# Performance work log

Hardware: AMD Instinct MI355X
Metric: run time of the kernel (lower is better)

The kernel has to match this reference:

```python
import jax, jax.numpy as jnp
import numpy as np

KERNEL = 2
STRIDE = 2
N_QUBITS = 4
N_LAYERS = 2
PI = np.float32(np.pi)
EPS = np.float32(1e-8)


def setup_inputs() -> dict:
    key = jax.random.key(0)
    k1, k2, k3, k4 = jax.random.split(key, 4)
    x = jax.random.normal(k1, (64, 3, 512, 512), dtype=jnp.float32)
    weights = jax.random.normal(k2, (N_LAYERS, N_QUBITS, 3), dtype=jnp.float32) * 0.1
    proj_w = jax.random.normal(k3, (4, N_QUBITS, 1, 1), dtype=jnp.float32) * 0.5
    proj_b = jax.random.normal(k4, (4,), dtype=jnp.float32) * 0.1
    return {"x": x, "weights": weights, "proj_w": proj_w, "proj_b": proj_b}


def _extract_patches(x):
    # x: (B, C, H, W) -> flattened 2x2 patches of grayscale image: (B, Ho, Wo, 4)
    B, C, H, W = x.shape
    Ho = (H - KERNEL) // STRIDE + 1
    Wo = (W - KERNEL) // STRIDE + 1
    x_gray = x.mean(axis=1)  # (B, H, W)
    # stride == kernel, so non-overlapping patches via reshape
    p = x_gray.reshape(B, Ho, KERNEL, Wo, KERNEL)
    p = p.transpose(0, 1, 3, 2, 4).reshape(B, Ho, Wo, KERNEL * KERNEL)
    return p


def reference(x, weights, proj_w, proj_b):
    patches = _extract_patches(x)  # (B, Ho, Wo, 4)
    # global min-max normalization (matches patches.min()/max() over whole tensor)
    pmin = patches.min()
    pmax = patches.max()
    patches = (patches - pmin) / (pmax - pmin + EPS)

    # simplified quantum simulation, fully vectorized over (B, Ho, Wo)
    encoded = jnp.sin(patches * PI)  # (B, Ho, Wo, Q)
    for layer in range(N_LAYERS):
        w = weights[layer]  # (Q, 3)
        neighbor = jnp.roll(encoded, shift=-1, axis=-1)  # encoded[(i+1)%Q]
        mixed = encoded * jnp.cos(w[:, 0]) + neighbor * jnp.sin(w[:, 1]) + w[:, 2]
        encoded = jnp.tanh(mixed)

    # (B, Ho, Wo, Q) -> (B, Q, Ho, Wo), then 1x1 conv projection
    q = encoded.transpose(0, 3, 1, 2)
    out = jnp.einsum('bqhw,oq->bohw', q, proj_w[:, :, 0, 0]) + proj_b[None, :, None, None]
    return out
```

## Files before the change

### kernel.cpp

```cpp
#include <hip/hip_runtime.h>
#include <hip/hip_fp16.h>

constexpr int BN = 64, CH = 3, HH = 512, WW = 512;
constexpr int HO = 256, WO = 256;
constexpr int HW = HH * WW;
constexpr int HOWO = HO * WO;
constexpr float EPS_F = 1e-8f;

constexpr int TPB = 256;
constexpr int GROUPS = BN * HO * (WO / 4);
constexpr int ABLOCKS = 2048;
constexpr int AT = ABLOCKS * TPB;
constexpr int AITERS = GROUPS / AT;
constexpr int CBLOCKS = GROUPS / TPB;

constexpr size_t GRAY_HALFS = (size_t)GROUPS * 16;

__device__ __forceinline__ float fast_tanh(float x) {
    float t = __builtin_amdgcn_exp2f(x * 2.8853900817779268f);
    return 1.0f - 2.0f * __builtin_amdgcn_rcpf(t + 1.0f);
}

__global__ __launch_bounds__(TPB) void k_pass1(const float* __restrict__ x,
                                               float4* __restrict__ gray4,
                                               float* __restrict__ part) {
    const int tid = blockIdx.x * TPB + threadIdx.x;
    const float c13 = 1.0f / 3.0f;
    float vmin = __int_as_float(0x7F800000);
    float vmax = __int_as_float(0xFF800000);

    #pragma unroll
    for (int it = 0; it < AITERS; ++it) {
        int grp = it * AT + tid;
        int b   = grp >> 14;
        int rem = grp & 16383;
        int ho  = rem >> 6;
        int wp  = rem & 63;
        const float* base = x + b * (CH * HW) + (2 * ho) * WW + 8 * wp;

        float row0[8], row1[8];
        #pragma unroll
        for (int c = 0; c < CH; ++c) {
            const float* pc = base + c * HW;
            float4 u0 = *(const float4*)(pc);
            float4 u1 = *(const float4*)(pc + 4);
            float4 v0 = *(const float4*)(pc + WW);
            float4 v1 = *(const float4*)(pc + WW + 4);
            float uu[8] = {u0.x, u0.y, u0.z, u0.w, u1.x, u1.y, u1.z, u1.w};
            float vv[8] = {v0.x, v0.y, v0.z, v0.w, v1.x, v1.y, v1.z, v1.w};
            if (c == 0) {
                #pragma unroll
                for (int k = 0; k < 8; ++k) { row0[k] = uu[k]; row1[k] = vv[k]; }
            } else {
                #pragma unroll
                for (int k = 0; k < 8; ++k) { row0[k] += uu[k]; row1[k] += vv[k]; }
            }
        }
        #pragma unroll
        for (int k = 0; k < 8; ++k) {
            row0[k] *= c13; row1[k] *= c13;
            vmin = fminf(vmin, fminf(row0[k], row1[k]));
            vmax = fmaxf(vmax, fmaxf(row0[k], row1[k]));
        }
        alignas(16) __half2 h2[8];
        #pragma unroll
        for (int p = 0; p < 4; ++p) {
            h2[2 * p]     = __floats2half2_rn(row0[2 * p], row0[2 * p + 1]);
            h2[2 * p + 1] = __floats2half2_rn(row1[2 * p], row1[2 * p + 1]);
        }
        gray4[(size_t)grp * 2]     = *(const float4*)&h2[0];
        gray4[(size_t)grp * 2 + 1] = *(const float4*)&h2[4];
    }

    #pragma unroll
    for (int off = 32; off > 0; off >>= 1) {
        vmin = fminf(vmin, __shfl_down(vmin, off, 64));
        vmax = fmaxf(vmax, __shfl_down(vmax, off, 64));
    }
    __shared__ float sm[8];
    int lane = threadIdx.x & 63, wid = threadIdx.x >> 6;
    if (lane == 0) { sm[wid] = vmin; sm[4 + wid] = vmax; }
    __syncthreads();
    if (threadIdx.x == 0) {
        part[2 * blockIdx.x]     = fminf(fminf(sm[0], sm[1]), fminf(sm[2], sm[3]));
        part[2 * blockIdx.x + 1] = fmaxf(fmaxf(sm[4], sm[5]), fmaxf(sm[6], sm[7]));
    }
}

__global__ __launch_bounds__(TPB) void k_reduce(const float* __restrict__ part,
                                                float* __restrict__ mm) {
    float m = __int_as_float(0x7F800000);
    float M = __int_as_float(0xFF800000);
    #pragma unroll
    for (int i = 0; i < ABLOCKS / TPB; ++i) {
        int j = i * TPB + threadIdx.x;
        m = fminf(m, part[2 * j]);
        M = fmaxf(M, part[2 * j + 1]);
    }
    #pragma unroll
    for (int off = 32; off > 0; off >>= 1) {
        m = fminf(m, __shfl_down(m, off, 64));
        M = fmaxf(M, __shfl_down(M, off, 64));
    }
    __shared__ float sm[8];
    int lane = threadIdx.x & 63, wid = threadIdx.x >> 6;
    if (lane == 0) { sm[wid] = m; sm[4 + wid] = M; }
    __syncthreads();
    if (threadIdx.x == 0) {
        mm[0] = fminf(fminf(sm[0], sm[1]), fminf(sm[2], sm[3]));
        mm[1] = fmaxf(fmaxf(sm[4], sm[5]), fmaxf(sm[6], sm[7]));
    }
}

__global__ __launch_bounds__(TPB) void k_main(const float4* __restrict__ gray4,
                                              const float* __restrict__ wts,
                                              const float* __restrict__ pw,
                                              const float* __restrict__ pb,
                                              const float* __restrict__ mm,
                                              float* __restrict__ out) {
    int grp = blockIdx.x * TPB + threadIdx.x;
    int b   = grp >> 14;
    int rem = grp & 16383;
    int ho  = rem >> 6;
    int wp  = rem & 63;

    float pmin   = mm[0];
    float sscale = 0.5f / (mm[1] - pmin + EPS_F);

    const float inv2pi = 0.15915494309189535f;
    float c0[2][4], s1[2][4], b2[2][4];
    #pragma unroll
    for (int l = 0; l < 2; ++l)
        #pragma unroll
        for (int q = 0; q < 4; ++q) {
            c0[l][q] = __builtin_amdgcn_cosf(wts[(l * 4 + q) * 3 + 0] * inv2pi);
            s1[l][q] = __builtin_amdgcn_sinf(wts[(l * 4 + q) * 3 + 1] * inv2pi);
            b2[l][q] = wts[(l * 4 + q) * 3 + 2];
        }
    float pwr[4][4], pbr[4];
    #pragma unroll
    for (int o = 0; o < 4; ++o) {
        pbr[o] = pb[o];
        #pragma unroll
        for (int q = 0; q < 4; ++q) pwr[o][q] = pw[o * 4 + q];
    }

    alignas(16) __half2 h2[8];
    *(float4*)&h2[0] = gray4[(size_t)grp * 2];
    *(float4*)&h2[4] = gray4[(size_t)grp * 2 + 1];

    float e[4][4];
    #pragma unroll
    for (int p = 0; p < 4; ++p) {
        e[p][0] = __low2float(h2[2 * p]);     e[p][1] = __high2float(h2[2 * p]);
        e[p][2] = __low2float(h2[2 * p + 1]); e[p][3] = __high2float(h2[2 * p + 1]);
    }
    #pragma unroll
    for (int p = 0; p < 4; ++p)
        #pragma unroll
        for (int q = 0; q < 4; ++q)
            e[p][q] = __builtin_amdgcn_sinf((e[p][q] - pmin) * sscale);
    #pragma unroll
    for (int l = 0; l < 2; ++l)
        #pragma unroll
        for (int p = 0; p < 4; ++p) {
            float mq[4];
            #pragma unroll
            for (int q = 0; q < 4; ++q)
                mq[q] = e[p][q] * c0[l][q] + e[p][(q + 1) & 3] * s1[l][q] + b2[l][q];
            #pragma unroll
            for (int q = 0; q < 4; ++q) e[p][q] = fast_tanh(mq[q]);
        }

    float* ob = out + b * (4 * HOWO) + ho * WO + 4 * wp;
    #pragma unroll
    for (int o = 0; o < 4; ++o) {
        float4 v;
        float* vp = &v.x;
        #pragma unroll
        for (int p = 0; p < 4; ++p) {
            float acc = pbr[o];
            #pragma unroll
            for (int q = 0; q < 4; ++q) acc += e[p][q] * pwr[o][q];
            vp[p] = acc;
        }
        *(float4*)(ob + o * HOWO) = v;
    }
}

extern "C" void kernel_launch(void* const* d_in, const int* in_sizes, int n_in,
                              void* d_out, int out_size, void* d_ws, size_t ws_size,
                              hipStream_t stream) {
    const float* x   = (const float*)d_in[0];
    const float* wts = (const float*)d_in[1];
    const float* pw  = (const float*)d_in[2];
    const float* pb  = (const float*)d_in[3];
    float* out = (float*)d_out;

    float4* gray4 = (float4*)d_ws;
    float*  part  = (float*)((char*)d_ws + GRAY_HALFS * sizeof(__half));
    float*  mm    = part + 2 * ABLOCKS;

    k_pass1 <<<ABLOCKS, TPB, 0, stream>>>(x, gray4, part);
    k_reduce<<<1,       TPB, 0, stream>>>(part, mm);
    k_main  <<<CBLOCKS, TPB, 0, stream>>>(gray4, wts, pw, pb, mm, out);
}
```

Measured before the change: 313.3 us.

## Fuse all passes into one cooperative persistent kernel holding gray values in registers

Replaces the three-kernel pipeline with a single cooperative kernel of 1024 blocks. Each thread keeps its fp16 grayscale patches in registers across a grid-wide sync, then finishes the global min/max reduction and computes the output. This removes the round trip of the grayscale intermediate through global memory and two kernel launches. The costs are higher register pressure (FITERS=4 groups of 8 half2 per thread), a grid barrier, and needing all 1024 blocks co-resident; the old three-kernel path is kept as a fallback if the cooperative launch fails.

```diff
diff --git a/kernel.cpp b/kernel.cpp
--- a/kernel.cpp
+++ b/kernel.cpp
@@ -1,5 +1,8 @@
 #include <hip/hip_runtime.h>
 #include <hip/hip_fp16.h>
+#include <hip/hip_cooperative_groups.h>
+
+namespace cg = cooperative_groups;
 
 constexpr int BN = 64, CH = 3, HH = 512, WW = 512;
 constexpr int HO = 256, WO = 256;
@@ -9,16 +12,174 @@
 
 constexpr int TPB = 256;
 constexpr int GROUPS = BN * HO * (WO / 4);
+
+constexpr int FBLK = 1024;
+constexpr int FTHR = FBLK * TPB;
+constexpr int FITERS = GROUPS / FTHR;
+
 constexpr int ABLOCKS = 2048;
 constexpr int AT = ABLOCKS * TPB;
 constexpr int AITERS = GROUPS / AT;
 constexpr int CBLOCKS = GROUPS / TPB;
-
 constexpr size_t GRAY_HALFS = (size_t)GROUPS * 16;
 
 __device__ __forceinline__ float fast_tanh(float x) {
     float t = __builtin_amdgcn_exp2f(x * 2.8853900817779268f);
     return 1.0f - 2.0f * __builtin_amdgcn_rcpf(t + 1.0f);
+}
+
+__global__ __launch_bounds__(TPB, 4) void k_fused(const float* __restrict__ x,
+                                                  const float* __restrict__ wts,
+                                                  const float* __restrict__ pw,
+                                                  const float* __restrict__ pb,
+                                                  float* __restrict__ part,
+                                                  float* __restrict__ out) {
+    const int tid = blockIdx.x * TPB + threadIdx.x;
+    const float c13 = 1.0f / 3.0f;
+    float vmin = __int_as_float(0x7F800000);
+    float vmax = __int_as_float(0xFF800000);
+
+    __half2 g[FITERS][8];
+
+    #pragma unroll
+    for (int it = 0; it < FITERS; ++it) {
+        const int grp = it * FTHR + tid;
+        const int b   = grp >> 14;
+        const int rem = grp & 16383;
+        const int ho  = rem >> 6;
+        const int wp  = rem & 63;
+        const float* base = x + b * (CH * HW) + (2 * ho) * WW + 8 * wp;
+
+        float row0[8], row1[8];
+        #pragma unroll
+        for (int c = 0; c < CH; ++c) {
+            const float* pc = base + c * HW;
+            float4 u0 = *(const float4*)(pc);
+            float4 u1 = *(const float4*)(pc + 4);
+            float4 v0 = *(const float4*)(pc + WW);
+            float4 v1 = *(const float4*)(pc + WW + 4);
+            float uu[8] = {u0.x, u0.y, u0.z, u0.w, u1.x, u1.y, u1.z, u1.w};
+            float vv[8] = {v0.x, v0.y, v0.z, v0.w, v1.x, v1.y, v1.z, v1.w};
+            if (c == 0) {
+                #pragma unroll
+                for (int k = 0; k < 8; ++k) { row0[k] = uu[k]; row1[k] = vv[k]; }
+            } else {
+                #pragma unroll
+                for (int k = 0; k < 8; ++k) { row0[k] += uu[k]; row1[k] += vv[k]; }
+            }
+        }
+        #pragma unroll
+        for (int k = 0; k < 8; ++k) {
+            row0[k] *= c13; row1[k] *= c13;
+            vmin = fminf(vmin, fminf(row0[k], row1[k]));
+            vmax = fmaxf(vmax, fmaxf(row0[k], row1[k]));
+        }
+        #pragma unroll
+        for (int p = 0; p < 4; ++p) {
+            g[it][2 * p]     = __floats2half2_rn(row0[2 * p], row0[2 * p + 1]);
+            g[it][2 * p + 1] = __floats2half2_rn(row1[2 * p], row1[2 * p + 1]);
+        }
+    }
+
+    #pragma unroll
+    for (int off = 32; off > 0; off >>= 1) {
+        vmin = fminf(vmin, __shfl_down(vmin, off, 64));
+        vmax = fmaxf(vmax, __shfl_down(vmax, off, 64));
+    }
+    __shared__ float sm[8];
+    const int lane = threadIdx.x & 63, wid = threadIdx.x >> 6;
+    if (lane == 0) { sm[wid] = vmin; sm[4 + wid] = vmax; }
+    __syncthreads();
+    if (threadIdx.x == 0) {
+        part[2 * blockIdx.x]     = fminf(fminf(sm[0], sm[1]), fminf(sm[2], sm[3]));
+        part[2 * blockIdx.x + 1] = fmaxf(fmaxf(sm[4], sm[5]), fmaxf(sm[6], sm[7]));
+    }
+
+    cg::this_grid().sync();
+
+    float m = __int_as_float(0x7F800000);
+    float M = __int_as_float(0xFF800000);
+    #pragma unroll
+    for (int i = 0; i < FBLK / TPB; ++i) {
+        const int j = i * TPB + threadIdx.x;
+        m = fminf(m, part[2 * j]);
+        M = fmaxf(M, part[2 * j + 1]);
+    }
+    #pragma unroll
+    for (int off = 32; off > 0; off >>= 1) {
+        m = fminf(m, __shfl_down(m, off, 64));
+        M = fmaxf(M, __shfl_down(M, off, 64));
+    }
+    if (lane == 0) { sm[wid] = m; sm[4 + wid] = M; }
+    __syncthreads();
+    const float pmin = fminf(fminf(sm[0], sm[1]), fminf(sm[2], sm[3]));
+    const float pmax = fmaxf(fmaxf(sm[4], sm[5]), fmaxf(sm[6], sm[7]));
+    const float sscale = 0.5f / (pmax - pmin + EPS_F);
+
+    const float inv2pi = 0.15915494309189535f;
+    float c0[2][4], s1[2][4], b2[2][4];
+    #pragma unroll
+    for (int l = 0; l < 2; ++l)
+        #pragma unroll
+        for (int q = 0; q < 4; ++q) {
+            c0[l][q] = __builtin_amdgcn_cosf(wts[(l * 4 + q) * 3 + 0] * inv2pi);
+            s1[l][q] = __builtin_amdgcn_sinf(wts[(l * 4 + q) * 3 + 1] * inv2pi);
+            b2[l][q] = wts[(l * 4 + q) * 3 + 2];
+        }
+    float pwr[4][4], pbr[4];
+    #pragma unroll
+    for (int o = 0; o < 4; ++o) {
+        pbr[o] = pb[o];
+        #pragma unroll
+        for (int q = 0; q < 4; ++q) pwr[o][q] = pw[o * 4 + q];
+    }
+
+    #pragma unroll
+    for (int it = 0; it < FITERS; ++it) {
+        const int grp = it * FTHR + tid;
+        const int b   = grp >> 14;
+        const int rem = grp & 16383;
+        const int ho  = rem >> 6;
+        const int wp  = rem & 63;
+
+        float e[4][4];
+        #pragma unroll
+        for (int p = 0; p < 4; ++p) {
+            e[p][0] = __low2float(g[it][2 * p]);     e[p][1] = __high2float(g[it][2 * p]);
+            e[p][2] = __low2float(g[it][2 * p + 1]); e[p][3] = __high2float(g[it][2 * p + 1]);
+        }
+        #pragma unroll
+        for (int p = 0; p < 4; ++p)
+            #pragma unroll
+            for (int q = 0; q < 4; ++q)
+                e[p][q] = __builtin_amdgcn_sinf((e[p][q] - pmin) * sscale);
+        #pragma unroll
+        for (int l = 0; l < 2; ++l)
+            #pragma unroll
+            for (int p = 0; p < 4; ++p) {
+                float mq[4];
+                #pragma unroll
+                for (int q = 0; q < 4; ++q)
+                    mq[q] = e[p][q] * c0[l][q] + e[p][(q + 1) & 3] * s1[l][q] + b2[l][q];
+                #pragma unroll
+                for (int q = 0; q < 4; ++q) e[p][q] = fast_tanh(mq[q]);
+            }
+
+        float* ob = out + b * (4 * HOWO) + ho * WO + 4 * wp;
+        #pragma unroll
+        for (int o = 0; o < 4; ++o) {
+            float4 v;
+            float* vp = &v.x;
+            #pragma unroll
+            for (int p = 0; p < 4; ++p) {
+                float acc = pbr[o];
+                #pragma unroll
+                for (int q = 0; q < 4; ++q) acc += e[p][q] * pwr[o][q];
+                vp[p] = acc;
+            }
+            *(float4*)(ob + o * HOWO) = v;
+        }
+    }
 }
 
 __global__ __launch_bounds__(TPB) void k_pass1(const float* __restrict__ x,
@@ -195,13 +356,19 @@
     const float* wts = (const float*)d_in[1];
     const float* pw  = (const float*)d_in[2];
     const float* pb  = (const float*)d_in[3];
-    float* out = (float*)d_out;
-
-    float4* gray4 = (float4*)d_ws;
-    float*  part  = (float*)((char*)d_ws + GRAY_HALFS * sizeof(__half));
-    float*  mm    = part + 2 * ABLOCKS;
-
-    k_pass1 <<<ABLOCKS, TPB, 0, stream>>>(x, gray4, part);
-    k_reduce<<<1,       TPB, 0, stream>>>(part, mm);
-    k_main  <<<CBLOCKS, TPB, 0, stream>>>(gray4, wts, pw, pb, mm, out);
-}
+    float* out  = (float*)d_out;
+    float* part = (float*)d_ws;
+
+    void* args[] = {(void*)&x, (void*)&wts, (void*)&pw, (void*)&pb,
+                    (void*)&part, (void*)&out};
+    hipError_t err = hipLaunchCooperativeKernel((const void*)k_fused, dim3(FBLK),
+                                                dim3(TPB), args, 0, stream);
+    if (err != hipSuccess) {
+        float4* gray4 = (float4*)d_ws;
+        float*  fpart = (float*)((char*)d_ws + GRAY_HALFS * sizeof(__half));
+        float*  mm    = fpart + 2 * ABLOCKS;
+        k_pass1 <<<ABLOCKS, TPB, 0, stream>>>(x, gray4, fpart);
+        k_reduce<<<1,       TPB, 0, stream>>>(fpart, mm);
+        k_main  <<<CBLOCKS, TPB, 0, stream>>>(gray4, wts, pw, pb, mm, out);
+    }
+}
```

Measured after the change: 440.1 us. 40.5% more time.
